# Optimization experiments

Measured on AMD Instinct MI355X. Metric: run time of the kernel, lower is better.

Reference implementation:

```python
import jax, jax.numpy as jnp
import numpy as np

N = 65536      # H*W pixels (256x256)
S = 1024       # superpixels
C = 128        # input channels
HIDE = 128     # hidden width
OUT = 64       # per-branch width (hide//2, concat=True)
CLS = 16       # classes
E_A = 16384    # superpixel adjacency edges
E_IMP = 6144   # importance (k=6) edges
E_PX = 1048576 # pixel row/col mask edges
EPS = 1e-5


def setup_inputs() -> dict:
    key = jax.random.key(0)
    ks = iter(jax.random.split(key, 64))
    nrm = lambda shape: jax.random.normal(next(ks), shape, dtype=jnp.float32) * 0.05
    uni = lambda shape, lo=0.0, hi=1.0: jax.random.uniform(next(ks), shape, dtype=jnp.float32, minval=lo, maxval=hi)
    ridx = lambda shape, hi: jax.random.randint(next(ks), shape, 0, hi, dtype=jnp.int32)
    d = {}
    d['x'] = jax.random.normal(next(ks), (N, C), dtype=jnp.float32)
    d['Q'] = uni((N, S))
    d['prelin_w'] = nrm((C, HIDE)); d['prelin_b'] = jnp.zeros((HIDE,), jnp.float32)
    d['bn0_g'] = jnp.ones((HIDE,), jnp.float32); d['bn0_b'] = jnp.zeros((HIDE,), jnp.float32)
    d['bn0_m'] = nrm((HIDE,)); d['bn0_v'] = uni((HIDE,), 0.5, 1.5)
    d['mmpn_w'] = nrm((5, HIDE, HIDE)); d['mmpn_b'] = jnp.zeros((5, HIDE), jnp.float32)
    d['mmpn_bn_g'] = jnp.ones((5, HIDE), jnp.float32); d['mmpn_bn_b'] = jnp.zeros((5, HIDE), jnp.float32)
    d['mmpn_bn_m'] = nrm((5, HIDE)); d['mmpn_bn_v'] = uni((5, HIDE), 0.5, 1.5)
    d['A_val'] = uni((E_A,)); d['imp_val'] = uni((E_IMP,))
    d['px_rowv_w'] = nrm((2, HIDE, OUT)); d['px_rowv_b'] = jnp.zeros((2, OUT), jnp.float32)
    d['px_colv_w'] = nrm((2, HIDE, OUT)); d['px_colv_b'] = jnp.zeros((2, OUT), jnp.float32)
    d['px_rowq_w'] = nrm((2, HIDE, OUT)); d['px_rowq_b'] = jnp.zeros((2, OUT), jnp.float32)
    d['px_colq_w'] = nrm((2, HIDE, OUT)); d['px_colq_b'] = jnp.zeros((2, OUT), jnp.float32)
    d['px_bn_g'] = jnp.ones((2, HIDE), jnp.float32); d['px_bn_b'] = jnp.zeros((2, HIDE), jnp.float32)
    d['px_bn_m'] = nrm((2, HIDE)); d['px_bn_v'] = uni((2, HIDE), 0.5, 1.5)
    d['final_w'] = nrm((HIDE, CLS)); d['final_b'] = jnp.zeros((CLS,), jnp.float32)
    d['A_src'] = ridx((E_A,), S); d['A_dst'] = ridx((E_A,), S)
    d['imp_src'] = ridx((E_IMP,), S); d['imp_dst'] = ridx((E_IMP,), S)
    d['row_src'] = ridx((E_PX,), N); d['row_dst'] = ridx((E_PX,), N)
    d['col_src'] = ridx((E_PX,), N); d['col_dst'] = ridx((E_PX,), N)
    return d


def _bn(x, g, b, m, v):
    # BatchNorm1d, eval mode (running stats)
    return g * (x - m) * jax.lax.rsqrt(v + EPS) + b


def _lrelu(x):
    return jnp.where(x >= 0, x, 0.01 * x)


def _ln(x):
    # F.layer_norm without affine params
    mu = jnp.mean(x, axis=-1, keepdims=True)
    var = jnp.mean(jnp.square(x - mu), axis=-1, keepdims=True)
    return (x - mu) * jax.lax.rsqrt(var + EPS)


def _seg_softmax(scores, ids, n):
    m = jax.ops.segment_max(scores, ids, num_segments=n)
    e = jnp.exp(scores - m[ids])
    d = jax.ops.segment_sum(e, ids, num_segments=n)
    return e / d[ids]


def _forward(x, Q, prelin_w, prelin_b, bn0_g, bn0_b, bn0_m, bn0_v,
             mmpn_w, mmpn_b, mmpn_bn_g, mmpn_bn_b, mmpn_bn_m, mmpn_bn_v,
             A_val, imp_val,
             px_rowv_w, px_rowv_b, px_colv_w, px_colv_b,
             px_rowq_w, px_rowq_b, px_colq_w, px_colq_b,
             px_bn_g, px_bn_b, px_bn_m, px_bn_v,
             final_w, final_b,
             A_src, A_dst, imp_src, imp_dst, row_src, row_dst, col_src, col_dst):
    x0 = _bn(x @ prelin_w + prelin_b, bn0_g, bn0_b, bn0_m, bn0_v)  # [N, HIDE]

    # ---- Hyperpixel_MMPN branch ----
    ncQ = Q / jnp.sum(Q, axis=0, keepdims=True)       # column-normalized Q
    hp = ncQ.T @ x0                                    # [S, HIDE]
    for i in range(5):
        h = hp @ mmpn_w[i] + mmpn_b[i]
        agg = jax.ops.segment_sum(A_val[:, None] * h[A_src], A_dst, num_segments=S)
        agg = agg + jax.ops.segment_sum(imp_val[:, None] * hp[imp_src], imp_dst, num_segments=S)
        hp = _lrelu(_bn(agg, mmpn_bn_g[i], mmpn_bn_b[i], mmpn_bn_m[i], mmpn_bn_v[i]))
    hyp = Q @ hp                                       # [N, HIDE]

    # ---- Pixel sparse-former branch ----
    px = x0
    for j in range(2):
        rowv = px @ px_rowv_w[j] + px_rowv_b[j]        # [N, OUT]
        colv = px @ px_colv_w[j] + px_colv_b[j]
        rowQ = _ln(px @ px_rowq_w[j] + px_rowq_b[j])
        colQ = _ln(px @ px_colq_w[j] + px_colq_b[j])
        rs = jnp.sum(rowQ[row_src] * rowQ[row_dst], axis=1) / OUT
        cs = jnp.sum(colQ[col_src] * colQ[col_dst], axis=1) / OUT
        ra = _seg_softmax(rs, row_src, N)
        ca = _seg_softmax(cs, col_src, N)
        rowout = jax.ops.segment_sum(rowv[row_dst] * ra[:, None], row_src, num_segments=N)
        colout = jax.ops.segment_sum(colv[col_dst] * ca[:, None], col_src, num_segments=N)
        out = jnp.concatenate((rowout, colout), axis=1)  # [N, HIDE]
        px = _lrelu(_bn(out, px_bn_g[j], px_bn_b[j], px_bn_m[j], px_bn_v[j]))

    H1 = hyp + px
    return jax.nn.softmax(H1 @ final_w + final_b, axis=-1)


def reference(x, Q, prelin_w, prelin_b, bn0_g, bn0_b, bn0_m, bn0_v,
              mmpn_w, mmpn_b, mmpn_bn_g, mmpn_bn_b, mmpn_bn_m, mmpn_bn_v,
              A_val, imp_val,
              px_rowv_w, px_rowv_b, px_colv_w, px_colv_b,
              px_rowq_w, px_rowq_b, px_colq_w, px_colq_b,
              px_bn_g, px_bn_b, px_bn_m, px_bn_v,
              final_w, final_b,
              A_src, A_dst, imp_src, imp_dst, row_src, row_dst, col_src, col_dst):
    return _forward(x, Q, prelin_w, prelin_b, bn0_g, bn0_b, bn0_m, bn0_v,
                    mmpn_w, mmpn_b, mmpn_bn_g, mmpn_bn_b, mmpn_bn_m, mmpn_bn_v,
                    A_val, imp_val,
                    px_rowv_w, px_rowv_b, px_colv_w, px_colv_b,
                    px_rowq_w, px_rowq_b, px_colq_w, px_colq_b,
                    px_bn_g, px_bn_b, px_bn_m, px_bn_v,
                    final_w, final_b,
                    A_src, A_dst, imp_src, imp_dst, row_src, row_dst, col_src, col_dst)
```

## Files before the change

kernel.cpp:

```cpp
#include <hip/hip_runtime.h>
#include <math.h>

#define N_PIX 65536
#define S_SP  1024
#define C_IN  128
#define HIDE  128
#define OUTW  64
#define NCLS  16
#define E_A   16384
#define E_IMP 6144
#define E_PX  1048576
#define EPSV  1e-5f

typedef __attribute__((ext_vector_type(4))) float f32x4;
typedef __attribute__((ext_vector_type(8))) short bf16x8;

__device__ inline ushort f2bf(float f) {
  uint u = __builtin_bit_cast(uint, f);
  uint r = (u + 0x7FFFu + ((u >> 16) & 1u)) >> 16;
  return (ushort)r;
}

__global__ __launch_bounds__(256) void k_x0(
    const float* __restrict__ x, const float* __restrict__ W,
    const float* __restrict__ bias, const float* __restrict__ g,
    const float* __restrict__ bb, const float* __restrict__ m,
    const float* __restrict__ vv, float* __restrict__ out) {
  __shared__ float Wl[128 * 128];
  __shared__ float Xl[32 * 128];
  int t = threadIdx.x;
  int n0 = blockIdx.x * 32;
  {
    const float4* Wg = (const float4*)W;
    float4* Wd = (float4*)Wl;
#pragma unroll
    for (int i = 0; i < 16; ++i) Wd[t + 256 * i] = Wg[t + 256 * i];
    const float4* Xg = (const float4*)(x + (size_t)n0 * 128);
    float4* Xd = (float4*)Xl;
#pragma unroll
    for (int i = 0; i < 4; ++i) Xd[t + 256 * i] = Xg[t + 256 * i];
  }
  __syncthreads();
  int ht = t & 31, nt = t >> 5;
  int h0 = ht * 4, r0 = nt * 4;
  float acc[4][4];
#pragma unroll
  for (int c = 0; c < 4; ++c) {
    float bv = bias[h0 + c];
#pragma unroll
    for (int r = 0; r < 4; ++r) acc[r][c] = bv;
  }
  for (int k = 0; k < 128; k += 4) {
    float4 xr[4], wk[4];
#pragma unroll
    for (int r = 0; r < 4; ++r) xr[r] = *(const float4*)&Xl[(r0 + r) * 128 + k];
#pragma unroll
    for (int kk = 0; kk < 4; ++kk) wk[kk] = *(const float4*)&Wl[(k + kk) * 128 + h0];
#pragma unroll
    for (int r = 0; r < 4; ++r) {
      float xs[4] = {xr[r].x, xr[r].y, xr[r].z, xr[r].w};
#pragma unroll
      for (int kk = 0; kk < 4; ++kk) {
        acc[r][0] += xs[kk] * wk[kk].x;
        acc[r][1] += xs[kk] * wk[kk].y;
        acc[r][2] += xs[kk] * wk[kk].z;
        acc[r][3] += xs[kk] * wk[kk].w;
      }
    }
  }
#pragma unroll
  for (int c = 0; c < 4; ++c) {
    int h = h0 + c;
    float sc = g[h] * rsqrtf(vv[h] + EPSV);
    float mb = m[h], bo = bb[h];
#pragma unroll
    for (int r = 0; r < 4; ++r) acc[r][c] = sc * (acc[r][c] - mb) + bo;
  }
#pragma unroll
  for (int r = 0; r < 4; ++r) {
    *(float4*)&out[(size_t)(n0 + r0 + r) * 128 + h0] =
        make_float4(acc[r][0], acc[r][1], acc[r][2], acc[r][3]);
  }
}

__global__ __launch_bounds__(256) void k_cast(
    const float* __restrict__ Q, ushort* __restrict__ Qt,
    float* __restrict__ csum) {
  __shared__ ushort Ot[64 * 258];
  __shared__ float Cs[64];
  int t = threadIdx.x;
  int nt = blockIdx.x & 255, st = blockIdx.x >> 8;
  int n0 = nt * 256, s0 = st * 64;
  int lr = t & 15, lg = t >> 4;
  if (t < 64) Cs[t] = 0.f;
  __syncthreads();
  float sums[4] = {0.f, 0.f, 0.f, 0.f};
#pragma unroll
  for (int nb = 0; nb < 4; ++nb) {
    ushort hh[4][4];
#pragma unroll
    for (int u = 0; u < 4; ++u) {
      int n = n0 + nb * 64 + lg * 4 + u;
      float4 q = *(const float4*)&Q[(size_t)n * 1024 + s0 + lr * 4];
      sums[0] += q.x; sums[1] += q.y; sums[2] += q.z; sums[3] += q.w;
      hh[u][0] = f2bf(q.x); hh[u][1] = f2bf(q.y);
      hh[u][2] = f2bf(q.z); hh[u][3] = f2bf(q.w);
    }
#pragma unroll
    for (int v = 0; v < 4; ++v) {
      uint lo = (uint)hh[0][v] | ((uint)hh[1][v] << 16);
      uint hi = (uint)hh[2][v] | ((uint)hh[3][v] << 16);
      ushort* p = &Ot[(lr * 4 + v) * 258 + nb * 64 + lg * 4];
      *(uint*)p = lo;
      *(uint*)(p + 2) = hi;
    }
  }
#pragma unroll
  for (int v = 0; v < 4; ++v) atomicAdd(&Cs[lr * 4 + v], sums[v]);
  __syncthreads();
  if (t < 64) atomicAdd(&csum[s0 + t], Cs[t]);
#pragma unroll
  for (int i = 0; i < 16; ++i) {
    int v2 = i * 256 + t;
    int s_loc = v2 >> 6, nq = v2 & 63;
    const ushort* p = &Ot[s_loc * 258 + nq * 4];
    uint2 o;
    o.x = *(const uint*)p;
    o.y = *(const uint*)(p + 2);
    *(uint2*)&Qt[(size_t)(s0 + s_loc) * 65536 + n0 + nq * 4] = o;
  }
}

__global__ __launch_bounds__(256) void k_xT(
    const float* __restrict__ x0, ushort* __restrict__ x0T) {
  __shared__ ushort Ot[128 * 258];
  int t = threadIdx.x;
  int n0 = blockIdx.x * 256;
  int lr = t & 31, lg = t >> 5;
#pragma unroll
  for (int nb = 0; nb < 8; ++nb) {
    ushort hh[4][4];
#pragma unroll
    for (int u = 0; u < 4; ++u) {
      int n = n0 + nb * 32 + lg * 4 + u;
      float4 q = *(const float4*)&x0[(size_t)n * 128 + lr * 4];
      hh[u][0] = f2bf(q.x); hh[u][1] = f2bf(q.y);
      hh[u][2] = f2bf(q.z); hh[u][3] = f2bf(q.w);
    }
#pragma unroll
    for (int v = 0; v < 4; ++v) {
      uint lo = (uint)hh[0][v] | ((uint)hh[1][v] << 16);
      uint hi = (uint)hh[2][v] | ((uint)hh[3][v] << 16);
      ushort* p = &Ot[(lr * 4 + v) * 258 + nb * 32 + lg * 4];
      *(uint*)p = lo;
      *(uint*)(p + 2) = hi;
    }
  }
  __syncthreads();
#pragma unroll
  for (int i = 0; i < 32; ++i) {
    int v2 = i * 256 + t;
    int h = v2 >> 6, nq = v2 & 63;
    const ushort* p = &Ot[h * 258 + nq * 4];
    uint2 o;
    o.x = *(const uint*)p;
    o.y = *(const uint*)(p + 2);
    *(uint2*)&x0T[(size_t)h * 65536 + n0 + nq * 4] = o;
  }
}

__global__ __launch_bounds__(256) void k_hpT(
    const float* __restrict__ hp, ushort* __restrict__ hpT) {
  __shared__ ushort Ot[128 * 258];
  int t = threadIdx.x;
  int s0 = blockIdx.x * 256;
  int lr = t & 31, lg = t >> 5;
#pragma unroll
  for (int sb = 0; sb < 8; ++sb) {
    ushort hh[4][4];
#pragma unroll
    for (int u = 0; u < 4; ++u) {
      int s = s0 + sb * 32 + lg * 4 + u;
      float4 q = *(const float4*)&hp[(size_t)s * 128 + lr * 4];
      hh[u][0] = f2bf(q.x); hh[u][1] = f2bf(q.y);
      hh[u][2] = f2bf(q.z); hh[u][3] = f2bf(q.w);
    }
#pragma unroll
    for (int v = 0; v < 4; ++v) {
      uint lo = (uint)hh[0][v] | ((uint)hh[1][v] << 16);
      uint hi = (uint)hh[2][v] | ((uint)hh[3][v] << 16);
      ushort* p = &Ot[(lr * 4 + v) * 258 + sb * 32 + lg * 4];
      *(uint*)p = lo;
      *(uint*)(p + 2) = hi;
    }
  }
  __syncthreads();
#pragma unroll
  for (int i = 0; i < 32; ++i) {
    int v2 = i * 256 + t;
    int h = v2 >> 6, sq = v2 & 63;
    const ushort* p = &Ot[h * 258 + sq * 4];
    uint2 o;
    o.x = *(const uint*)p;
    o.y = *(const uint*)(p + 2);
    *(uint2*)&hpT[(size_t)h * 1024 + s0 + sq * 4] = o;
  }
}

__global__ __launch_bounds__(256) void k_hpu(
    const ushort* __restrict__ Qt, const ushort* __restrict__ x0T,
    float* __restrict__ hp_part) {
  __shared__ ushort Al[256 * 72];
  __shared__ ushort Bl[128 * 72];
  int t = threadIdx.x;
  int mt = blockIdx.x & 3;
  int kb = blockIdx.x >> 2;
  int s_base = mt * 256;
  int n_base = kb * 1024;
  int wv = t >> 6, lane = t & 63;
  int lr = lane & 15, lq = lane >> 4;
  f32x4 acc[4][8];
#pragma unroll
  for (int i = 0; i < 4; ++i)
#pragma unroll
    for (int j = 0; j < 8; ++j) acc[i][j] = (f32x4){0.f, 0.f, 0.f, 0.f};
  for (int c = 0; c < 16; ++c) {
    int nc = n_base + c * 64;
#pragma unroll
    for (int i = 0; i < 8; ++i) {
      int v = i * 256 + t;
      int r = v >> 3, sg = v & 7;
      *(uint4*)&Al[r * 72 + sg * 8] =
          *(const uint4*)&Qt[(size_t)(s_base + r) * 65536 + nc + sg * 8];
    }
#pragma unroll
    for (int i = 0; i < 4; ++i) {
      int v = i * 256 + t;
      int r = v >> 3, sg = v & 7;
      *(uint4*)&Bl[r * 72 + sg * 8] =
          *(const uint4*)&x0T[(size_t)r * 65536 + nc + sg * 8];
    }
    __syncthreads();
#pragma unroll
    for (int kh = 0; kh < 2; ++kh) {
      bf16x8 af[4], bfr[8];
#pragma unroll
      for (int i = 0; i < 4; ++i)
        af[i] = *(const bf16x8*)&Al[(wv * 64 + i * 16 + lr) * 72 + kh * 32 + lq * 8];
#pragma unroll
      for (int j = 0; j < 8; ++j)
        bfr[j] = *(const bf16x8*)&Bl[(j * 16 + lr) * 72 + kh * 32 + lq * 8];
#pragma unroll
      for (int i = 0; i < 4; ++i)
#pragma unroll
        for (int j = 0; j < 8; ++j)
          acc[i][j] = __builtin_amdgcn_mfma_f32_16x16x32_bf16(af[i], bfr[j],
                                                              acc[i][j], 0, 0, 0);
    }
    __syncthreads();
  }
  float* outp = hp_part + (size_t)kb * 131072;
#pragma unroll
  for (int i = 0; i < 4; ++i) {
    int s_g = s_base + wv * 64 + i * 16 + lq * 4;
#pragma unroll
    for (int j = 0; j < 8; ++j) {
      int h = j * 16 + lr;
#pragma unroll
      for (int r = 0; r < 4; ++r)
        outp[(size_t)(s_g + r) * 128 + h] = acc[i][j][r];
    }
  }
}

__global__ void k_hpred(const float* __restrict__ part,
                        const float* __restrict__ csum, float* __restrict__ hp) {
  int tid = blockIdx.x * 256 + threadIdx.x;
  float s = 0.f;
  for (int kb = 0; kb < 64; ++kb) s += part[(size_t)kb * 131072 + tid];
  hp[tid] = s / csum[tid >> 7];
}

__global__ __launch_bounds__(256) void k_hyp(
    const float* __restrict__ Q, const ushort* __restrict__ hpT,
    float* __restrict__ hyp) {
  __shared__ ushort Al[256 * 72];
  __shared__ ushort Bl[128 * 72];
  int t = threadIdx.x;
  int n_base = blockIdx.x * 256;
  int wv = t >> 6, lane = t & 63;
  int lr = lane & 15, lq = lane >> 4;
  f32x4 acc[4][8];
#pragma unroll
  for (int i = 0; i < 4; ++i)
#pragma unroll
    for (int j = 0; j < 8; ++j) acc[i][j] = (f32x4){0.f, 0.f, 0.f, 0.f};
  for (int c = 0; c < 16; ++c) {
    int sc = c * 64;
#pragma unroll
    for (int i = 0; i < 16; ++i) {
      int v = i * 256 + t;
      int r = v >> 4, sq = v & 15;
      float4 f = *(const float4*)&Q[(size_t)(n_base + r) * 1024 + sc + sq * 4];
      uint2 pk;
      pk.x = (uint)f2bf(f.x) | ((uint)f2bf(f.y) << 16);
      pk.y = (uint)f2bf(f.z) | ((uint)f2bf(f.w) << 16);
      *(uint2*)&Al[r * 72 + sq * 4] = pk;
    }
#pragma unroll
    for (int i = 0; i < 4; ++i) {
      int v = i * 256 + t;
      int r = v >> 3, sg = v & 7;
      *(uint4*)&Bl[r * 72 + sg * 8] =
          *(const uint4*)&hpT[(size_t)r * 1024 + sc + sg * 8];
    }
    __syncthreads();
#pragma unroll
    for (int kh = 0; kh < 2; ++kh) {
      bf16x8 af[4], bfr[8];
#pragma unroll
      for (int i = 0; i < 4; ++i)
        af[i] = *(const bf16x8*)&Al[(wv * 64 + i * 16 + lr) * 72 + kh * 32 + lq * 8];
#pragma unroll
      for (int j = 0; j < 8; ++j)
        bfr[j] = *(const bf16x8*)&Bl[(j * 16 + lr) * 72 + kh * 32 + lq * 8];
#pragma unroll
      for (int i = 0; i < 4; ++i)
#pragma unroll
        for (int j = 0; j < 8; ++j)
          acc[i][j] = __builtin_amdgcn_mfma_f32_16x16x32_bf16(af[i], bfr[j],
                                                              acc[i][j], 0, 0, 0);
    }
    __syncthreads();
  }
#pragma unroll
  for (int i = 0; i < 4; ++i) {
    int n_g = n_base + wv * 64 + i * 16 + lq * 4;
#pragma unroll
    for (int j = 0; j < 8; ++j) {
      int h = j * 16 + lr;
#pragma unroll
      for (int r = 0; r < 4; ++r)
        hyp[(size_t)(n_g + r) * 128 + h] = acc[i][j][r];
    }
  }
}

__global__ __launch_bounds__(256) void k_slin(
    const float* __restrict__ A, const float* __restrict__ W,
    const float* __restrict__ bias, float* __restrict__ out) {
  __shared__ float Wl[128 * 128];
  __shared__ float Xl[32 * 128];
  int t = threadIdx.x;
  int n0 = blockIdx.x * 32;
  {
    const float4* Wg = (const float4*)W;
    float4* Wd = (float4*)Wl;
#pragma unroll
    for (int i = 0; i < 16; ++i) Wd[t + 256 * i] = Wg[t + 256 * i];
    const float4* Xg = (const float4*)(A + (size_t)n0 * 128);
    float4* Xd = (float4*)Xl;
#pragma unroll
    for (int i = 0; i < 4; ++i) Xd[t + 256 * i] = Xg[t + 256 * i];
  }
  __syncthreads();
  int ht = t & 31, nt = t >> 5;
  int h0 = ht * 4, r0 = nt * 4;
  float acc[4][4];
#pragma unroll
  for (int c = 0; c < 4; ++c) {
    float bv = bias[h0 + c];
#pragma unroll
    for (int r = 0; r < 4; ++r) acc[r][c] = bv;
  }
  for (int k = 0; k < 128; k += 4) {
    float4 xr[4], wk[4];
#pragma unroll
    for (int r = 0; r < 4; ++r) xr[r] = *(const float4*)&Xl[(r0 + r) * 128 + k];
#pragma unroll
    for (int kk = 0; kk < 4; ++kk) wk[kk] = *(const float4*)&Wl[(k + kk) * 128 + h0];
#pragma unroll
    for (int r = 0; r < 4; ++r) {
      float xs[4] = {xr[r].x, xr[r].y, xr[r].z, xr[r].w};
#pragma unroll
      for (int kk = 0; kk < 4; ++kk) {
        acc[r][0] += xs[kk] * wk[kk].x;
        acc[r][1] += xs[kk] * wk[kk].y;
        acc[r][2] += xs[kk] * wk[kk].z;
        acc[r][3] += xs[kk] * wk[kk].w;
      }
    }
  }
#pragma unroll
  for (int r = 0; r < 4; ++r) {
    *(float4*)&out[(size_t)(n0 + r0 + r) * 128 + h0] =
        make_float4(acc[r][0], acc[r][1], acc[r][2], acc[r][3]);
  }
}

__global__ void k_edge_mmpn(
    const float* __restrict__ htmp, const float* __restrict__ hp,
    const float* __restrict__ A_val, const int* __restrict__ A_src,
    const int* __restrict__ A_dst, const float* __restrict__ imp_val,
    const int* __restrict__ imp_src, const int* __restrict__ imp_dst,
    float* __restrict__ agg) {
  long tid = (long)blockIdx.x * 256 + threadIdx.x;
  if (tid < (long)E_A * HIDE) {
    int e = (int)(tid >> 7), h = (int)(tid & 127);
    atomicAdd(&agg[(size_t)A_dst[e] * HIDE + h],
              A_val[e] * htmp[(size_t)A_src[e] * HIDE + h]);
  } else {
    long t2 = tid - (long)E_A * HIDE;
    if (t2 < (long)E_IMP * HIDE) {
      int e = (int)(t2 >> 7), h = (int)(t2 & 127);
      atomicAdd(&agg[(size_t)imp_dst[e] * HIDE + h],
                imp_val[e] * hp[(size_t)imp_src[e] * HIDE + h]);
    }
  }
}

__global__ void k_mmpn_bn(const float* __restrict__ agg, const float* __restrict__ g,
                          const float* __restrict__ b, const float* __restrict__ m,
                          const float* __restrict__ v, float* __restrict__ hp) {
  int tid = blockIdx.x * 256 + threadIdx.x;
  int h = tid & 127;
  float sc = g[h] * rsqrtf(v[h] + EPSV);
  float y = sc * (agg[tid] - m[h]) + b[h];
  hp[tid] = y >= 0.f ? y : 0.01f * y;
}

__global__ __launch_bounds__(256) void k_pxlin(
    const float* __restrict__ px, const float* __restrict__ Wrv,
    const float* __restrict__ Wcv, const float* __restrict__ Wrq,
    const float* __restrict__ Wcq, const float* __restrict__ brv,
    const float* __restrict__ bcv, const float* __restrict__ brq,
    const float* __restrict__ bcq, float* __restrict__ out) {
  __shared__ float Xl[32 * 128];
  __shared__ float Wl[32 * 256];
  int t = threadIdx.x;
  int n0 = blockIdx.x * 32;
  {
    float4* Xd = (float4*)Xl;
    const float4* Xg = (const float4*)(px + (size_t)n0 * 128);
#pragma unroll
    for (int it = 0; it < 4; ++it) Xd[t + 256 * it] = Xg[t + 256 * it];
  }
  int ct = t & 63, nt = t >> 6;
  int c0 = ct * 4, r0 = nt * 8;
  float acc[8][4];
  {
    int mt = c0 >> 6, cb = c0 & 63;
    const float* bs = mt == 0 ? brv : mt == 1 ? bcv : mt == 2 ? brq : bcq;
#pragma unroll
    for (int c = 0; c < 4; ++c) {
      float bv = bs[cb + c];
#pragma unroll
      for (int r = 0; r < 8; ++r) acc[r][c] = bv;
    }
  }
  for (int kc = 0; kc < 4; ++kc) {
    int k0 = kc * 32;
    __syncthreads();
    {
#pragma unroll
      for (int it = 0; it < 8; ++it) {
        int v = t + 256 * it;
        int kk = v >> 6, cq = v & 63;
        int c = cq * 4;
        int mt = c >> 6, cb = c & 63;
        const float* Ws = mt == 0 ? Wrv : mt == 1 ? Wcv : mt == 2 ? Wrq : Wcq;
        *(float4*)&Wl[kk * 256 + c] = *(const float4*)&Ws[(size_t)(k0 + kk) * 64 + cb];
      }
    }
    __syncthreads();
    for (int k = 0; k < 32; k += 4) {
      float4 wq[4];
#pragma unroll
      for (int kk = 0; kk < 4; ++kk) wq[kk] = *(const float4*)&Wl[(k + kk) * 256 + c0];
#pragma unroll
      for (int r = 0; r < 8; ++r) {
        float4 xq = *(const float4*)&Xl[(r0 + r) * 128 + k0 + k];
        float xs[4] = {xq.x, xq.y, xq.z, xq.w};
#pragma unroll
        for (int kk = 0; kk < 4; ++kk) {
          acc[r][0] += xs[kk] * wq[kk].x;
          acc[r][1] += xs[kk] * wq[kk].y;
          acc[r][2] += xs[kk] * wq[kk].z;
          acc[r][3] += xs[kk] * wq[kk].w;
        }
      }
    }
  }
#pragma unroll
  for (int r = 0; r < 8; ++r) {
    *(float4*)&out[(size_t)(n0 + r0 + r) * 256 + c0] =
        make_float4(acc[r][0], acc[r][1], acc[r][2], acc[r][3]);
  }
}

__global__ void k_ln(float* __restrict__ lin4) {
  int row = blockIdx.x * 4 + (threadIdx.x >> 6);
  int lane = threadIdx.x & 63;
  float* p = lin4 + (size_t)row * 256;
#pragma unroll
  for (int g = 0; g < 2; ++g) {
    float v = p[128 + g * 64 + lane];
    float s = v, s2 = v * v;
#pragma unroll
    for (int o = 32; o > 0; o >>= 1) {
      s += __shfl_xor(s, o, 64);
      s2 += __shfl_xor(s2, o, 64);
    }
    float mu = s * (1.0f / 64.0f);
    float var = s2 * (1.0f / 64.0f) - mu * mu;
    p[128 + g * 64 + lane] = (v - mu) * rsqrtf(var + EPSV);
  }
}

__global__ void k_hist(const int* __restrict__ src, int* __restrict__ cnt) {
  int e = blockIdx.x * 256 + threadIdx.x;
  atomicAdd(&cnt[src[e]], 1);
}

__global__ __launch_bounds__(1024) void k_scan(const int* __restrict__ cnt,
                                               int* __restrict__ off,
                                               int* __restrict__ cur) {
  __shared__ int part[1024];
  int t = threadIdx.x;
  int base = t * 64;
  int s = 0;
  for (int i = 0; i < 64; ++i) s += cnt[base + i];
  part[t] = s;
  __syncthreads();
  for (int o = 1; o < 1024; o <<= 1) {
    int v = part[t];
    int add = (t >= o) ? part[t - o] : 0;
    __syncthreads();
    part[t] = v + add;
    __syncthreads();
  }
  int run = (t > 0) ? part[t - 1] : 0;
  for (int i = 0; i < 64; ++i) {
    off[base + i] = run;
    cur[base + i] = run;
    run += cnt[base + i];
  }
  if (t == 1023) off[65536] = run;
}

__global__ void k_fill(const int* __restrict__ src, const int* __restrict__ dst,
                       int* __restrict__ cur, int* __restrict__ csr) {
  int e = blockIdx.x * 256 + threadIdx.x;
  int p = atomicAdd(&cur[src[e]], 1);
  csr[p] = dst[e];
}

__global__ __launch_bounds__(256) void k_gather(
    const float* __restrict__ lin4, int qoff, int voff,
    const int* __restrict__ off, const int* __restrict__ csr_dst,
    float* __restrict__ outp, int ooff) {
  int node = blockIdx.x * 4 + (threadIdx.x >> 6);
  int l = threadIdx.x & 63;
  float qs = lin4[(size_t)node * 256 + qoff + l];
  int i0 = off[node], i1 = off[node + 1];
  float acc = 0.f, den = 0.f;
  for (int i = i0; i < i1; ++i) {
    int d = csr_dst[i];
    const float* base = lin4 + (size_t)d * 256;
    float qd = base[qoff + l];
    float vd = base[voff + l];
    float p = qs * qd;
#pragma unroll
    for (int o = 32; o > 0; o >>= 1) p += __shfl_xor(p, o, 64);
    float w = __expf(p * (1.0f / OUTW));
    den += w;
    acc += w * vd;
  }
  float r = den > 0.f ? 1.0f / den : 0.f;
  outp[(size_t)node * HIDE + ooff + l] = acc * r;
}

__global__ void k_pxbn(float* __restrict__ px, const float* __restrict__ g,
                       const float* __restrict__ b, const float* __restrict__ m,
                       const float* __restrict__ v) {
  int tid = blockIdx.x * 256 + threadIdx.x;
  int h = tid & 127;
  float x = px[tid];
  float sc = g[h] * rsqrtf(v[h] + EPSV);
  float y = sc * (x - m[h]) + b[h];
  px[tid] = y >= 0.f ? y : 0.01f * y;
}

__global__ __launch_bounds__(256) void k_final(
    const float* __restrict__ hyp, const float* __restrict__ px,
    const float* __restrict__ W, const float* __restrict__ b,
    float* __restrict__ out) {
  __shared__ float Wl[128 * 16];
  __shared__ float rl[16 * 129];
  int t = threadIdx.x;
  int n0 = blockIdx.x * 16;
#pragma unroll
  for (int i = 0; i < 8; ++i) Wl[t + 256 * i] = W[t + 256 * i];
#pragma unroll
  for (int i = 0; i < 8; ++i) {
    int v = t + 256 * i;
    int r = v >> 7, c = v & 127;
    rl[r * 129 + c] = hyp[(size_t)(n0 + r) * 128 + c] + px[(size_t)(n0 + r) * 128 + c];
  }
  __syncthreads();
  int r = t >> 4, cls = t & 15;
  float acc = b[cls];
  for (int k = 0; k < 128; ++k) acc += rl[r * 129 + k] * Wl[k * 16 + cls];
  float mx = acc;
#pragma unroll
  for (int o = 8; o > 0; o >>= 1) mx = fmaxf(mx, __shfl_xor(mx, o, 16));
  float e = expf(acc - mx), s = e;
#pragma unroll
  for (int o = 8; o > 0; o >>= 1) s += __shfl_xor(s, o, 16);
  out[(size_t)(n0 + r) * 16 + cls] = e / s;
}

extern "C" void kernel_launch(void* const* d_in, const int* in_sizes, int n_in,
                              void* d_out, int out_size, void* d_ws, size_t ws_size,
                              hipStream_t stream) {
  const float* x        = (const float*)d_in[0];
  const float* Q        = (const float*)d_in[1];
  const float* prelin_w = (const float*)d_in[2];
  const float* prelin_b = (const float*)d_in[3];
  const float* bn0_g    = (const float*)d_in[4];
  const float* bn0_b    = (const float*)d_in[5];
  const float* bn0_m    = (const float*)d_in[6];
  const float* bn0_v    = (const float*)d_in[7];
  const float* mmpn_w   = (const float*)d_in[8];
  const float* mmpn_b   = (const float*)d_in[9];
  const float* mmpn_bn_g= (const float*)d_in[10];
  const float* mmpn_bn_b= (const float*)d_in[11];
  const float* mmpn_bn_m= (const float*)d_in[12];
  const float* mmpn_bn_v= (const float*)d_in[13];
  const float* A_val    = (const float*)d_in[14];
  const float* imp_val  = (const float*)d_in[15];
  const float* px_rowv_w= (const float*)d_in[16];
  const float* px_rowv_b= (const float*)d_in[17];
  const float* px_colv_w= (const float*)d_in[18];
  const float* px_colv_b= (const float*)d_in[19];
  const float* px_rowq_w= (const float*)d_in[20];
  const float* px_rowq_b= (const float*)d_in[21];
  const float* px_colq_w= (const float*)d_in[22];
  const float* px_colq_b= (const float*)d_in[23];
  const float* px_bn_g  = (const float*)d_in[24];
  const float* px_bn_b  = (const float*)d_in[25];
  const float* px_bn_m  = (const float*)d_in[26];
  const float* px_bn_v  = (const float*)d_in[27];
  const float* final_w  = (const float*)d_in[28];
  const float* final_b  = (const float*)d_in[29];
  const int* A_src   = (const int*)d_in[30];
  const int* A_dst   = (const int*)d_in[31];
  const int* imp_src = (const int*)d_in[32];
  const int* imp_dst = (const int*)d_in[33];
  const int* row_src = (const int*)d_in[34];
  const int* row_dst = (const int*)d_in[35];
  const int* col_src = (const int*)d_in[36];
  const int* col_dst = (const int*)d_in[37];
  float* out = (float*)d_out;

  float* ws = (float*)d_ws;
  float* x0px = ws; ws += (size_t)N_PIX * HIDE;
  float* hyp  = ws; ws += (size_t)N_PIX * HIDE;
  float* hp_part = hyp;
  float* big  = ws; ws += (size_t)32 * 1024 * 1024;
  ushort* Qt  = (ushort*)big;
  float* lin4 = big;
  int* off_row = (int*)(big + (size_t)N_PIX * 256);
  int* off_col = off_row + 65537;
  int* csr_row = off_col + 65537;
  int* csr_col = csr_row + E_PX;
  ushort* x0T = (ushort*)ws; ws += (size_t)HIDE * N_PIX / 2;
  ushort* hpT = (ushort*)ws; ws += (size_t)HIDE * S_SP / 2;
  float* csum = ws; ws += S_SP;
  float* hp   = ws; ws += (size_t)S_SP * HIDE;
  float* htmp = ws; ws += (size_t)S_SP * HIDE;
  float* agg  = ws; ws += (size_t)S_SP * HIDE;

  int* cnt_row = (int*)agg;
  int* cnt_col = (int*)agg + 65536;
  int* cur_row = (int*)htmp;
  int* cur_col = (int*)htmp + 65536;

  hipMemsetAsync(csum, 0, S_SP * sizeof(float), stream);

  k_cast<<<4096, 256, 0, stream>>>(Q, Qt, csum);
  k_x0<<<N_PIX / 32, 256, 0, stream>>>(x, prelin_w, prelin_b, bn0_g, bn0_b, bn0_m,
                                       bn0_v, x0px);
  k_xT<<<N_PIX / 256, 256, 0, stream>>>(x0px, x0T);
  k_hpu<<<256, 256, 0, stream>>>(Qt, x0T, hp_part);
  k_hpred<<<S_SP * HIDE / 256, 256, 0, stream>>>(hp_part, csum, hp);

  for (int i = 0; i < 5; ++i) {
    k_slin<<<S_SP / 32, 256, 0, stream>>>(hp, mmpn_w + (size_t)i * HIDE * HIDE,
                                          mmpn_b + i * HIDE, htmp);
    hipMemsetAsync(agg, 0, (size_t)S_SP * HIDE * sizeof(float), stream);
    k_edge_mmpn<<<(E_A + E_IMP) * HIDE / 256, 256, 0, stream>>>(
        htmp, hp, A_val, A_src, A_dst, imp_val, imp_src, imp_dst, agg);
    k_mmpn_bn<<<S_SP * HIDE / 256, 256, 0, stream>>>(
        agg, mmpn_bn_g + i * HIDE, mmpn_bn_b + i * HIDE, mmpn_bn_m + i * HIDE,
        mmpn_bn_v + i * HIDE, hp);
  }

  k_hpT<<<S_SP / 256, 256, 0, stream>>>(hp, hpT);
  k_hyp<<<N_PIX / 256, 256, 0, stream>>>(Q, hpT, hyp);

  hipMemsetAsync(cnt_row, 0, 2 * 65536 * sizeof(int), stream);
  k_hist<<<E_PX / 256, 256, 0, stream>>>(row_src, cnt_row);
  k_hist<<<E_PX / 256, 256, 0, stream>>>(col_src, cnt_col);
  k_scan<<<1, 1024, 0, stream>>>(cnt_row, off_row, cur_row);
  k_scan<<<1, 1024, 0, stream>>>(cnt_col, off_col, cur_col);
  k_fill<<<E_PX / 256, 256, 0, stream>>>(row_src, row_dst, cur_row, csr_row);
  k_fill<<<E_PX / 256, 256, 0, stream>>>(col_src, col_dst, cur_col, csr_col);

  for (int j = 0; j < 2; ++j) {
    k_pxlin<<<N_PIX / 32, 256, 0, stream>>>(
        x0px, px_rowv_w + j * 8192, px_colv_w + j * 8192, px_rowq_w + j * 8192,
        px_colq_w + j * 8192, px_rowv_b + j * 64, px_colv_b + j * 64,
        px_rowq_b + j * 64, px_colq_b + j * 64, lin4);
    k_ln<<<N_PIX / 4, 256, 0, stream>>>(lin4);
    k_gather<<<N_PIX / 4, 256, 0, stream>>>(lin4, 128, 0, off_row, csr_row, x0px, 0);
    k_gather<<<N_PIX / 4, 256, 0, stream>>>(lin4, 192, 64, off_col, csr_col, x0px, 64);
    k_pxbn<<<N_PIX * HIDE / 256, 256, 0, stream>>>(x0px, px_bn_g + j * HIDE,
                                                   px_bn_b + j * HIDE,
                                                   px_bn_m + j * HIDE,
                                                   px_bn_v + j * HIDE);
  }

  k_final<<<N_PIX / 16, 256, 0, stream>>>(hyp, x0px, final_w, final_b, out);
}
```

Measured before the change: 1.941 ms.

## Double-buffer and retile the Q GEMMs and reuse a cached bf16 copy of Q

Both Q GEMMs (superpixel pooling and the hyp projection) move to 128x128 tiles with a 2x2 wave layout. Global loads for the next K chunk are prefetched into registers and staged in a second LDS buffer, so loads overlap the MFMA work and only one barrier is needed per chunk. The pooling kernel now launches twice as many blocks. The cast kernel can also write a row-major bf16 copy of Q when the workspace has room, letting the hyp GEMM read half the bytes and skip the per-tile conversion. The cost is an extra 128MB write in the cast pass, and the fast path depends on workspace size.

```diff
diff --git a/kernel.cpp b/kernel.cpp
--- a/kernel.cpp
+++ b/kernel.cpp
@@ -85,7 +85,7 @@
 
 __global__ __launch_bounds__(256) void k_cast(
     const float* __restrict__ Q, ushort* __restrict__ Qt,
-    float* __restrict__ csum) {
+    float* __restrict__ csum, ushort* __restrict__ Qbf) {
   __shared__ ushort Ot[64 * 258];
   __shared__ float Cs[64];
   int t = threadIdx.x;
@@ -105,6 +105,12 @@
       sums[0] += q.x; sums[1] += q.y; sums[2] += q.z; sums[3] += q.w;
       hh[u][0] = f2bf(q.x); hh[u][1] = f2bf(q.y);
       hh[u][2] = f2bf(q.z); hh[u][3] = f2bf(q.w);
+      if (Qbf) {
+        uint2 w;
+        w.x = (uint)hh[u][0] | ((uint)hh[u][1] << 16);
+        w.y = (uint)hh[u][2] | ((uint)hh[u][3] << 16);
+        *(uint2*)&Qbf[(size_t)n * 1024 + s0 + lr * 4] = w;
+      }
     }
 #pragma unroll
     for (int v = 0; v < 4; ++v) {
@@ -207,65 +213,86 @@
   }
 }
 
-__global__ __launch_bounds__(256) void k_hpu(
+__device__ __forceinline__ void mfma_tile128(const ushort* Al, const ushort* Bl,
+                                             f32x4 acc[4][4], int wr, int wc,
+                                             int lr, int lq) {
+#pragma unroll
+  for (int kh = 0; kh < 2; ++kh) {
+    bf16x8 af[4], bf[4];
+#pragma unroll
+    for (int i = 0; i < 4; ++i)
+      af[i] = *(const bf16x8*)&Al[(wr * 64 + i * 16 + lr) * 72 + kh * 32 + lq * 8];
+#pragma unroll
+    for (int j = 0; j < 4; ++j)
+      bf[j] = *(const bf16x8*)&Bl[(wc * 64 + j * 16 + lr) * 72 + kh * 32 + lq * 8];
+#pragma unroll
+    for (int i = 0; i < 4; ++i)
+#pragma unroll
+      for (int j = 0; j < 4; ++j)
+        acc[i][j] = __builtin_amdgcn_mfma_f32_16x16x32_bf16(af[i], bf[j],
+                                                            acc[i][j], 0, 0, 0);
+  }
+}
+
+__global__ __launch_bounds__(256) void k_hpu2(
     const ushort* __restrict__ Qt, const ushort* __restrict__ x0T,
     float* __restrict__ hp_part) {
-  __shared__ ushort Al[256 * 72];
-  __shared__ ushort Bl[128 * 72];
-  int t = threadIdx.x;
-  int mt = blockIdx.x & 3;
-  int kb = blockIdx.x >> 2;
-  int s_base = mt * 256;
-  int n_base = kb * 1024;
+  __shared__ ushort Al[2][128 * 72];
+  __shared__ ushort Bl[2][128 * 72];
+  int t = threadIdx.x;
+  int st = blockIdx.x & 7, kb = blockIdx.x >> 3;
+  int s0 = st * 128;
   int wv = t >> 6, lane = t & 63;
+  int wr = wv >> 1, wc = wv & 1;
   int lr = lane & 15, lq = lane >> 4;
-  f32x4 acc[4][8];
+  int sr = t >> 3, sg = t & 7;
+  const ushort* Ab = Qt + (size_t)(s0 + sr) * 65536 + (size_t)kb * 1024 + sg * 8;
+  const ushort* Bb = x0T + (size_t)sr * 65536 + (size_t)kb * 1024 + sg * 8;
+  f32x4 acc[4][4];
 #pragma unroll
   for (int i = 0; i < 4; ++i)
 #pragma unroll
-    for (int j = 0; j < 8; ++j) acc[i][j] = (f32x4){0.f, 0.f, 0.f, 0.f};
+    for (int j = 0; j < 4; ++j) acc[i][j] = (f32x4){0.f, 0.f, 0.f, 0.f};
+  uint4 ra[4], rb[4];
+#pragma unroll
+  for (int i = 0; i < 4; ++i) {
+    ra[i] = *(const uint4*)(Ab + (size_t)i * 32 * 65536);
+    rb[i] = *(const uint4*)(Bb + (size_t)i * 32 * 65536);
+  }
+#pragma unroll
+  for (int i = 0; i < 4; ++i) {
+    *(uint4*)&Al[0][(sr + 32 * i) * 72 + sg * 8] = ra[i];
+    *(uint4*)&Bl[0][(sr + 32 * i) * 72 + sg * 8] = rb[i];
+  }
+  __syncthreads();
   for (int c = 0; c < 16; ++c) {
-    int nc = n_base + c * 64;
-#pragma unroll
-    for (int i = 0; i < 8; ++i) {
-      int v = i * 256 + t;
-      int r = v >> 3, sg = v & 7;
-      *(uint4*)&Al[r * 72 + sg * 8] =
-          *(const uint4*)&Qt[(size_t)(s_base + r) * 65536 + nc + sg * 8];
-    }
-#pragma unroll
-    for (int i = 0; i < 4; ++i) {
-      int v = i * 256 + t;
-      int r = v >> 3, sg = v & 7;
-      *(uint4*)&Bl[r * 72 + sg * 8] =
-          *(const uint4*)&x0T[(size_t)r * 65536 + nc + sg * 8];
+    int p = c & 1;
+    if (c < 15) {
+      int ko = (c + 1) * 64;
+#pragma unroll
+      for (int i = 0; i < 4; ++i) {
+        ra[i] = *(const uint4*)(Ab + (size_t)i * 32 * 65536 + ko);
+        rb[i] = *(const uint4*)(Bb + (size_t)i * 32 * 65536 + ko);
+      }
+    }
+    mfma_tile128(Al[p], Bl[p], acc, wr, wc, lr, lq);
+    if (c < 15) {
+      int q = p ^ 1;
+#pragma unroll
+      for (int i = 0; i < 4; ++i) {
+        *(uint4*)&Al[q][(sr + 32 * i) * 72 + sg * 8] = ra[i];
+        *(uint4*)&Bl[q][(sr + 32 * i) * 72 + sg * 8] = rb[i];
+      }
     }
     __syncthreads();
-#pragma unroll
-    for (int kh = 0; kh < 2; ++kh) {
-      bf16x8 af[4], bfr[8];
-#pragma unroll
-      for (int i = 0; i < 4; ++i)
-        af[i] = *(const bf16x8*)&Al[(wv * 64 + i * 16 + lr) * 72 + kh * 32 + lq * 8];
-#pragma unroll
-      for (int j = 0; j < 8; ++j)
-        bfr[j] = *(const bf16x8*)&Bl[(j * 16 + lr) * 72 + kh * 32 + lq * 8];
-#pragma unroll
-      for (int i = 0; i < 4; ++i)
-#pragma unroll
-        for (int j = 0; j < 8; ++j)
-          acc[i][j] = __builtin_amdgcn_mfma_f32_16x16x32_bf16(af[i], bfr[j],
-                                                              acc[i][j], 0, 0, 0);
-    }
-    __syncthreads();
   }
   float* outp = hp_part + (size_t)kb * 131072;
 #pragma unroll
   for (int i = 0; i < 4; ++i) {
-    int s_g = s_base + wv * 64 + i * 16 + lq * 4;
-#pragma unroll
-    for (int j = 0; j < 8; ++j) {
-      int h = j * 16 + lr;
+    int s_g = s0 + wr * 64 + i * 16 + lq * 4;
+#pragma unroll
+    for (int j = 0; j < 4; ++j) {
+      int h = wc * 64 + j * 16 + lr;
 #pragma unroll
       for (int r = 0; r < 4; ++r)
         outp[(size_t)(s_g + r) * 128 + h] = acc[i][j][r];
@@ -281,64 +308,139 @@
   hp[tid] = s / csum[tid >> 7];
 }
 
-__global__ __launch_bounds__(256) void k_hyp(
+__global__ __launch_bounds__(256) void k_hyp_bf(
+    const ushort* __restrict__ Qbf, const ushort* __restrict__ hpT,
+    float* __restrict__ hyp) {
+  __shared__ ushort Al[2][128 * 72];
+  __shared__ ushort Bl[2][128 * 72];
+  int t = threadIdx.x;
+  int n0 = blockIdx.x * 128;
+  int wv = t >> 6, lane = t & 63;
+  int wr = wv >> 1, wc = wv & 1;
+  int lr = lane & 15, lq = lane >> 4;
+  int sr = t >> 3, sg = t & 7;
+  const ushort* Ab = Qbf + (size_t)(n0 + sr) * 1024 + sg * 8;
+  const ushort* Bb = hpT + (size_t)sr * 1024 + sg * 8;
+  f32x4 acc[4][4];
+#pragma unroll
+  for (int i = 0; i < 4; ++i)
+#pragma unroll
+    for (int j = 0; j < 4; ++j) acc[i][j] = (f32x4){0.f, 0.f, 0.f, 0.f};
+  uint4 ra[4], rb[4];
+#pragma unroll
+  for (int i = 0; i < 4; ++i) {
+    ra[i] = *(const uint4*)(Ab + (size_t)i * 32 * 1024);
+    rb[i] = *(const uint4*)(Bb + (size_t)i * 32 * 1024);
+  }
+#pragma unroll
+  for (int i = 0; i < 4; ++i) {
+    *(uint4*)&Al[0][(sr + 32 * i) * 72 + sg * 8] = ra[i];
+    *(uint4*)&Bl[0][(sr + 32 * i) * 72 + sg * 8] = rb[i];
+  }
+  __syncthreads();
+  for (int c = 0; c < 16; ++c) {
+    int p = c & 1;
+    if (c < 15) {
+      int ko = (c + 1) * 64;
+#pragma unroll
+      for (int i = 0; i < 4; ++i) {
+        ra[i] = *(const uint4*)(Ab + (size_t)i * 32 * 1024 + ko);
+        rb[i] = *(const uint4*)(Bb + (size_t)i * 32 * 1024 + ko);
+      }
+    }
+    mfma_tile128(Al[p], Bl[p], acc, wr, wc, lr, lq);
+    if (c < 15) {
+      int q = p ^ 1;
+#pragma unroll
+      for (int i = 0; i < 4; ++i) {
+        *(uint4*)&Al[q][(sr + 32 * i) * 72 + sg * 8] = ra[i];
+        *(uint4*)&Bl[q][(sr + 32 * i) * 72 + sg * 8] = rb[i];
+      }
+    }
+    __syncthreads();
+  }
+#pragma unroll
+  for (int i = 0; i < 4; ++i) {
+    int n_g = n0 + wr * 64 + i * 16 + lq * 4;
+#pragma unroll
+    for (int j = 0; j < 4; ++j) {
+      int h = wc * 64 + j * 16 + lr;
+#pragma unroll
+      for (int r = 0; r < 4; ++r)
+        hyp[(size_t)(n_g + r) * 128 + h] = acc[i][j][r];
+    }
+  }
+}
+
+__global__ __launch_bounds__(256) void k_hyp_f32(
     const float* __restrict__ Q, const ushort* __restrict__ hpT,
     float* __restrict__ hyp) {
-  __shared__ ushort Al[256 * 72];
-  __shared__ ushort Bl[128 * 72];
-  int t = threadIdx.x;
-  int n_base = blockIdx.x * 256;
+  __shared__ ushort Al[2][128 * 72];
+  __shared__ ushort Bl[2][128 * 72];
+  int t = threadIdx.x;
+  int n0 = blockIdx.x * 128;
   int wv = t >> 6, lane = t & 63;
+  int wr = wv >> 1, wc = wv & 1;
   int lr = lane & 15, lq = lane >> 4;
-  f32x4 acc[4][8];
+  int ar = t >> 4, ag = t & 15;
+  int sr = t >> 3, sg = t & 7;
+  const float* Af = Q + (size_t)(n0 + ar) * 1024 + ag * 4;
+  const ushort* Bb = hpT + (size_t)sr * 1024 + sg * 8;
+  f32x4 acc[4][4];
 #pragma unroll
   for (int i = 0; i < 4; ++i)
 #pragma unroll
-    for (int j = 0; j < 8; ++j) acc[i][j] = (f32x4){0.f, 0.f, 0.f, 0.f};
+    for (int j = 0; j < 4; ++j) acc[i][j] = (f32x4){0.f, 0.f, 0.f, 0.f};
+  float4 rf[8];
+  uint4 rb[4];
+#pragma unroll
+  for (int i = 0; i < 8; ++i) rf[i] = *(const float4*)(Af + (size_t)i * 16 * 1024);
+#pragma unroll
+  for (int i = 0; i < 4; ++i) rb[i] = *(const uint4*)(Bb + (size_t)i * 32 * 1024);
+#pragma unroll
+  for (int i = 0; i < 8; ++i) {
+    uint2 pk;
+    pk.x = (uint)f2bf(rf[i].x) | ((uint)f2bf(rf[i].y) << 16);
+    pk.y = (uint)f2bf(rf[i].z) | ((uint)f2bf(rf[i].w) << 16);
+    *(uint2*)&Al[0][(ar + 16 * i) * 72 + ag * 4] = pk;
+  }
+#pragma unroll
+  for (int i = 0; i < 4; ++i)
+    *(uint4*)&Bl[0][(sr + 32 * i) * 72 + sg * 8] = rb[i];
+  __syncthreads();
   for (int c = 0; c < 16; ++c) {
-    int sc = c * 64;
-#pragma unroll
-    for (int i = 0; i < 16; ++i) {
-      int v = i * 256 + t;
-      int r = v >> 4, sq = v & 15;
-      float4 f = *(const float4*)&Q[(size_t)(n_base + r) * 1024 + sc + sq * 4];
-      uint2 pk;
-      pk.x = (uint)f2bf(f.x) | ((uint)f2bf(f.y) << 16);
-      pk.y = (uint)f2bf(f.z) | ((uint)f2bf(f.w) << 16);
-      *(uint2*)&Al[r * 72 + sq * 4] = pk;
-    }
-#pragma unroll
-    for (int i = 0; i < 4; ++i) {
-      int v = i * 256 + t;
-      int r = v >> 3, sg = v & 7;
-      *(uint4*)&Bl[r * 72 + sg * 8] =
-          *(const uint4*)&hpT[(size_t)r * 1024 + sc + sg * 8];
+    int p = c & 1;
+    if (c < 15) {
+      int ko = (c + 1) * 64;
+#pragma unroll
+      for (int i = 0; i < 8; ++i)
+        rf[i] = *(const float4*)(Af + (size_t)i * 16 * 1024 + ko);
+#pragma unroll
+      for (int i = 0; i < 4; ++i)
+        rb[i] = *(const uint4*)(Bb + (size_t)i * 32 * 1024 + ko);
+    }
+    mfma_tile128(Al[p], Bl[p], acc, wr, wc, lr, lq);
+    if (c < 15) {
+      int q = p ^ 1;
+#pragma unroll
+      for (int i = 0; i < 8; ++i) {
+        uint2 pk;
+        pk.x = (uint)f2bf(rf[i].x) | ((uint)f2bf(rf[i].y) << 16);
+        pk.y = (uint)f2bf(rf[i].z) | ((uint)f2bf(rf[i].w) << 16);
+        *(uint2*)&Al[q][(ar + 16 * i) * 72 + ag * 4] = pk;
+      }
+#pragma unroll
+      for (int i = 0; i < 4; ++i)
+        *(uint4*)&Bl[q][(sr + 32 * i) * 72 + sg * 8] = rb[i];
     }
     __syncthreads();
-#pragma unroll
-    for (int kh = 0; kh < 2; ++kh) {
-      bf16x8 af[4], bfr[8];
-#pragma unroll
-      for (int i = 0; i < 4; ++i)
-        af[i] = *(const bf16x8*)&Al[(wv * 64 + i * 16 + lr) * 72 + kh * 32 + lq * 8];
-#pragma unroll
-      for (int j = 0; j < 8; ++j)
-        bfr[j] = *(const bf16x8*)&Bl[(j * 16 + lr) * 72 + kh * 32 + lq * 8];
-#pragma unroll
-      for (int i = 0; i < 4; ++i)
-#pragma unroll
-        for (int j = 0; j < 8; ++j)
-          acc[i][j] = __builtin_amdgcn_mfma_f32_16x16x32_bf16(af[i], bfr[j],
-                                                              acc[i][j], 0, 0, 0);
-    }
-    __syncthreads();
   }
 #pragma unroll
   for (int i = 0; i < 4; ++i) {
-    int n_g = n_base + wv * 64 + i * 16 + lq * 4;
-#pragma unroll
-    for (int j = 0; j < 8; ++j) {
-      int h = j * 16 + lr;
+    int n_g = n0 + wr * 64 + i * 16 + lq * 4;
+#pragma unroll
+    for (int j = 0; j < 4; ++j) {
+      int h = wc * 64 + j * 16 + lr;
 #pragma unroll
       for (int r = 0; r < 4; ++r)
         hyp[(size_t)(n_g + r) * 128 + h] = acc[i][j][r];
@@ -681,6 +783,11 @@
   float* htmp = ws; ws += (size_t)S_SP * HIDE;
   float* agg  = ws; ws += (size_t)S_SP * HIDE;
 
+  size_t used = (size_t)((char*)ws - (char*)d_ws);
+  ushort* Qbf = nullptr;
+  if (used + (size_t)N_PIX * S_SP * sizeof(ushort) <= ws_size)
+    Qbf = (ushort*)ws;
+
   int* cnt_row = (int*)agg;
   int* cnt_col = (int*)agg + 65536;
   int* cur_row = (int*)htmp;
@@ -688,11 +795,11 @@
 
   hipMemsetAsync(csum, 0, S_SP * sizeof(float), stream);
 
-  k_cast<<<4096, 256, 0, stream>>>(Q, Qt, csum);
+  k_cast<<<4096, 256, 0, stream>>>(Q, Qt, csum, Qbf);
   k_x0<<<N_PIX / 32, 256, 0, stream>>>(x, prelin_w, prelin_b, bn0_g, bn0_b, bn0_m,
                                        bn0_v, x0px);
   k_xT<<<N_PIX / 256, 256, 0, stream>>>(x0px, x0T);
-  k_hpu<<<256, 256, 0, stream>>>(Qt, x0T, hp_part);
+  k_hpu2<<<512, 256, 0, stream>>>(Qt, x0T, hp_part);
   k_hpred<<<S_SP * HIDE / 256, 256, 0, stream>>>(hp_part, csum, hp);
 
   for (int i = 0; i < 5; ++i) {
@@ -707,7 +814,10 @@
   }
 
   k_hpT<<<S_SP / 256, 256, 0, stream>>>(hp, hpT);
-  k_hyp<<<N_PIX / 256, 256, 0, stream>>>(Q, hpT, hyp);
+  if (Qbf)
+    k_hyp_bf<<<N_PIX / 128, 256, 0, stream>>>(Qbf, hpT, hyp);
+  else
+    k_hyp_f32<<<N_PIX / 128, 256, 0, stream>>>(Q, hpT, hyp);
 
   hipMemsetAsync(cnt_row, 0, 2 * 65536 * sizeof(int), stream);
   k_hist<<<E_PX / 256, 256, 0, stream>>>(row_src, cnt_row);
```

New measurement: 1.830 ms. 5.7% less time.
